# Kernel optimization log

Measured on AMD Instinct MI355X. Metric: run time of the kernel, lower is better.

## Reference

```python
import jax, jax.numpy as jnp
import numpy as np

EPS = 1e-5

def _quant_w(w):
    # symmetric per-tensor 8-bit weight quantization with straight-through estimator
    s = jnp.max(jnp.abs(w)) / 127.0
    wq = jnp.round(jnp.clip(w / s, -127.0, 127.0)) * s
    return w + jax.lax.stop_gradient(wq - w)

def _adder_conv(x, w, stride):
    # AdderNet conv: out[b,co,ow] = -sum_{cin,k} |x[b,cin,ow*stride+k] - w[co,cin,k]|
    # x: (B, Cin, L), w: (Co, Cin, K)
    B, Cin, L = x.shape
    Co, _, K = w.shape
    Ow = (L - K) // stride + 1
    idx = jnp.arange(Ow)[:, None] * stride + jnp.arange(K)[None, :]      # (Ow, K)
    patches = x[:, :, idx]                                               # (B, Cin, Ow, K)
    diff = jnp.abs(patches[:, None] - w[None, :, :, None, :])            # (B, Co, Cin, Ow, K)
    return -diff.sum(axis=(2, 4))                                        # (B, Co, Ow)

def _bn(x, p):
    # eval-mode BatchNorm; x: (B,C,W), p: (4,C) = [gamma, beta, running_mean, running_var]
    g, b, m, v = p
    return (x - m[:, None]) * (g[:, None] * jax.lax.rsqrt(v[:, None] + EPS)) + b[:, None]

def _bn_params(key, c):
    k1, k2, k3, k4 = jax.random.split(key, 4)
    g = jax.random.uniform(k1, (c,)) + 0.5
    b = 0.1 * jax.random.normal(k2, (c,))
    m = 0.1 * jax.random.normal(k3, (c,))
    v = jax.random.uniform(k4, (c,)) + 0.5
    return jnp.stack([g, b, m, v]).astype(jnp.float32)

def setup_inputs() -> dict:
    key = jax.random.key(0)
    ks = jax.random.split(key, 22)
    B = 8192
    w = lambda k, shp: (0.1 * jax.random.normal(k, shp)).astype(jnp.float32)
    return {
        'x': jax.random.normal(ks[0], (B, 1, 1, 256), dtype=jnp.float32),
        'w_pre1': w(ks[1], (5, 1, 13)),   'bn_pre1': _bn_params(ks[2], 5),
        'w_pre2': w(ks[3], (10, 5, 9)),   'bn_pre2': _bn_params(ks[4], 10),
        'w_r1':   w(ks[5], (10, 10, 1)),  'bn_r1':   _bn_params(ks[6], 10),
        'w_r2':   w(ks[7], (10, 10, 1)),  'bn_r2':   _bn_params(ks[8], 10),
        'w_o1a':  w(ks[9], (70, 140, 1)), 'bn_o1a':  _bn_params(ks[10], 70),
        'w_o1b':  w(ks[11], (30, 70, 1)), 'bn_o1b':  _bn_params(ks[12], 30),
        'w_o1c':  w(ks[13], (1, 30, 1)),  'bn_o1c':  _bn_params(ks[14], 1),
        'w_o2a':  w(ks[15], (70, 140, 1)),'bn_o2a':  _bn_params(ks[16], 70),
        'w_o2b':  w(ks[17], (30, 70, 1)), 'bn_o2b':  _bn_params(ks[18], 30),
        'w_o2c':  w(ks[19], (1, 30, 1)),  'bn_o2c':  _bn_params(ks[20], 1),
    }

def reference(x, w_pre1, bn_pre1, w_pre2, bn_pre2, w_r1, bn_r1, w_r2, bn_r2,
              w_o1a, bn_o1a, w_o1b, bn_o1b, w_o1c, bn_o1c,
              w_o2a, bn_o2a, w_o2b, bn_o2b, w_o2c, bn_o2c):
    relu = jax.nn.relu
    B = x.shape[0]
    h = x.reshape(B, 1, 256)                                  # height dim is 1 -> 1D
    h = relu(_bn(_adder_conv(h, _quant_w(w_pre1), 5), bn_pre1))   # (B,5,49)
    h = relu(_bn(_adder_conv(h, _quant_w(w_pre2), 3), bn_pre2))   # (B,10,14)
    # ResBlock
    t = relu(_bn(_adder_conv(h, _quant_w(w_r1), 1), bn_r1))
    t = _bn(_adder_conv(t, _quant_w(w_r2), 1), bn_r2)
    h = relu(t + h)                                           # (B,10,14)
    f = h.reshape(B, 140, 1)                                  # flatten to channels
    # O1 branch (amplitude-weighted average lifetime)
    a = relu(_bn(_adder_conv(f, _quant_w(w_o1a), 1), bn_o1a))
    a = relu(_bn(_adder_conv(a, _quant_w(w_o1b), 1), bn_o1b))
    a = relu(_bn(_adder_conv(a, _quant_w(w_o1c), 1), bn_o1c))
    tau_amp = a.reshape(-1)                                   # (B,)
    # O2 branch (intensity-weighted average lifetime)
    b = relu(_bn(_adder_conv(f, _quant_w(w_o2a), 1), bn_o2a))
    b = relu(_bn(_adder_conv(b, _quant_w(w_o2b), 1), bn_o2b))
    b = relu(_bn(_adder_conv(b, _quant_w(w_o2c), 1), bn_o2c))
    tau_inten = b.reshape(-1)                                 # (B,)
    return (tau_amp, tau_inten)
```

## Files before the change

### kernel.cpp

```cpp
#include <hip/hip_runtime.h>

#define TPB 256
#define EPB 8
#define H1S 246
#define ES  280

#define WQ1   0
#define WQ2   65
#define WR1Q  515
#define WR2Q  615
#define WCQ   715
#define WSB   779
#define SMALL_N 1253
#define WQAT  1280
#define WQBT  20880

#define SB_P1 0
#define SB_P2 10
#define SB_R1 30
#define SB_R2 50
#define SB_A1 70
#define SB_B1 210
#define SB_C1 270
#define SB_A2 272
#define SB_B2 412
#define SB_C2 472

#define GFOLD(bn, C, OFF)                                                     \
  if (tid < (C)) {                                                            \
    float gg = (bn)[tid], bb = (bn)[(C) + tid];                               \
    float mm = (bn)[2 * (C) + tid], vv = (bn)[3 * (C) + tid];                 \
    float sc = gg / sqrtf(vv + 1e-5f);                                        \
    sbp[(OFF) + tid] = sc;                                                    \
    sbp[(OFF) + (C) + tid] = bb - mm * sc;                                    \
  }

extern "C" __global__ __launch_bounds__(256)
void prep(const float* __restrict__ w1,  const float* __restrict__ bnp1,
          const float* __restrict__ w2,  const float* __restrict__ bnp2,
          const float* __restrict__ wr1, const float* __restrict__ bnr1,
          const float* __restrict__ wr2, const float* __restrict__ bnr2,
          const float* __restrict__ wa1, const float* __restrict__ bna1,
          const float* __restrict__ wb1, const float* __restrict__ bnb1,
          const float* __restrict__ wc1, const float* __restrict__ bnc1,
          const float* __restrict__ wa2, const float* __restrict__ bna2,
          const float* __restrict__ wb2, const float* __restrict__ bnb2,
          const float* __restrict__ wc2, const float* __restrict__ bnc2,
          float* __restrict__ ws)
{
  __shared__ float s_red[4];
  const int tid = threadIdx.x;
  const int b = blockIdx.x;

  if (b == 10) {
    float* sbp = ws + WSB;
    GFOLD(bnp1, 5, SB_P1)  GFOLD(bnp2, 10, SB_P2)
    GFOLD(bnr1, 10, SB_R1) GFOLD(bnr2, 10, SB_R2)
    GFOLD(bna1, 70, SB_A1) GFOLD(bnb1, 30, SB_B1) GFOLD(bnc1, 1, SB_C1)
    GFOLD(bna2, 70, SB_A2) GFOLD(bnb2, 30, SB_B2) GFOLD(bnc2, 1, SB_C2)
    return;
  }

  const float* src; int n; int mode; int rofs; float* dst = ws;
  int ofs = 0;
  switch (b) {
    case 0: src = w1;  ofs = WQ1;      n = 65;   mode = 0; rofs = 0;  break;
    case 1: src = w2;  ofs = WQ2;      n = 450;  mode = 0; rofs = 0;  break;
    case 2: src = wr1; ofs = WR1Q;     n = 100;  mode = 0; rofs = 0;  break;
    case 3: src = wr2; ofs = WR2Q;     n = 100;  mode = 0; rofs = 0;  break;
    case 4: src = wa1; ofs = WQAT;     n = 9800; mode = 1; rofs = 0;  break;
    case 5: src = wb1; ofs = WQBT;     n = 2100; mode = 2; rofs = 0;  break;
    case 6: src = wc1; ofs = WCQ;      n = 30;   mode = 0; rofs = 0;  break;
    case 7: src = wa2; ofs = WQAT;     n = 9800; mode = 1; rofs = 70; break;
    case 8: src = wb2; ofs = WQBT;     n = 2100; mode = 2; rofs = 30; break;
    default:src = wc2; ofs = WCQ + 32; n = 30;   mode = 0; rofs = 0;  break;
  }

  const int n4 = n >> 2;
  const float4* s4 = (const float4*)src;

  float m = 0.f;
  for (int i = tid; i < n4; i += 256) {
    float4 v = s4[i];
    m = fmaxf(m, fmaxf(fmaxf(fabsf(v.x), fabsf(v.y)),
                       fmaxf(fabsf(v.z), fabsf(v.w))));
  }
  for (int i = (n4 << 2) + tid; i < n; i += 256) m = fmaxf(m, fabsf(src[i]));
#pragma unroll
  for (int off = 32; off > 0; off >>= 1)
    m = fmaxf(m, __shfl_down(m, off, 64));
  if ((tid & 63) == 0) s_red[tid >> 6] = m;
  __syncthreads();
  m = fmaxf(fmaxf(s_red[0], s_red[1]), fmaxf(s_red[2], s_red[3]));

  const float s = m / 127.0f;
  auto qz = [&](float w) {
    return rintf(fminf(fmaxf(w / s, -127.f), 127.f)) * s;
  };

  if (mode == 0) {
    for (int i = tid; i < n4; i += 256) {
      float4 v = s4[i];
      int base = 4 * i;
      dst[ofs + base]     = qz(v.x);
      dst[ofs + base + 1] = qz(v.y);
      dst[ofs + base + 2] = qz(v.z);
      dst[ofs + base + 3] = qz(v.w);
    }
    for (int i = (n4 << 2) + tid; i < n; i += 256) dst[ofs + i] = qz(src[i]);
  } else if (mode == 1) {
    for (int i = tid; i < n4; i += 256) {
      float4 v = s4[i];
      int base = 4 * i;
      int r = base / 140 + rofs, c = base % 140;
      float4 q4;
      q4.x = qz(v.x); q4.y = qz(v.y); q4.z = qz(v.z); q4.w = qz(v.w);
      *(float4*)&dst[ofs + ((c >> 2) * 140 + r) * 4] = q4;
    }
  } else {
    for (int i = tid; i < n4; i += 256) {
      float4 v = s4[i];
      int base = 4 * i;
      float q[4] = {qz(v.x), qz(v.y), qz(v.z), qz(v.w)};
#pragma unroll
      for (int cpt = 0; cpt < 4; ++cpt) {
        int ii = base + cpt;
        int r = ii / 70 + rofs, c = ii % 70;
        dst[ofs + ((c >> 1) * 60 + r) * 2 + (c & 1)] = q[cpt];
      }
    }
  }
}

extern "C" __global__ __launch_bounds__(TPB, 4)
void taunet(const float* __restrict__ x, const float* __restrict__ ws,
            float* __restrict__ out, int B)
{
  __shared__ __align__(16) float s_h1[EPB * H1S];
  __shared__ __align__(16) float s_e[EPB * ES];
  __shared__ __align__(16) float s_small[SMALL_N];

  const int tid = threadIdx.x;
  const int g  = tid >> 5;
  const int l  = tid & 31;
  const int ln = tid & 63;
  const int wv = tid >> 6;
  const int gp = 2 * wv;
  const int elem = blockIdx.x * EPB + g;

  {
    const float4* w4p = (const float4*)ws;
    for (int i = ln; i < (SMALL_N >> 2); i += 64)
      *(float4*)&s_small[i * 4] = w4p[i];
    if (ln == 0) s_small[1252] = ws[1252];
  }

  {
    const float4* xb = (const float4*)x;
#pragma unroll
    for (int it = 0; it < 2; ++it) {
      int e = gp + it;
      int ge = blockIdx.x * EPB + e;
      if (ge < B) {
        float4 v = xb[ge * 64 + ln];
        *(float4*)&s_e[e * ES + ln * 4] = v;
      }
    }
  }

  const float* sb = &s_small[WSB];

  {
    const float* xe = &s_e[g * ES];
#pragma unroll
    for (int rep = 0; rep < 2; ++rep) {
      int p = l + 32 * rep;
      bool act = p < 49;
      int ps = act ? p : 0;
      float win[13];
#pragma unroll
      for (int k = 0; k < 13; ++k) win[k] = xe[5 * ps + k];
#pragma unroll
      for (int ci = 0; ci < 5; ++ci) {
        float a0 = 0.f, a1 = 0.f;
#pragma unroll
        for (int k = 0; k < 13; ++k) {
          float d = fabsf(win[k] - ws[WQ1 + ci * 13 + k]);
          if (k & 1) a1 += d; else a0 += d;
        }
        float v = fmaxf(fmaf(-(a0 + a1), ws[WSB + SB_P1 + ci],
                             ws[WSB + SB_P1 + 5 + ci]), 0.f);
        if (act) s_h1[g * H1S + ci * 49 + ps] = v;
      }
    }
  }

  {
    const int ch = l >> 4;
    const int ow16 = l & 15;
    const bool act = ow16 < 14;
    const int ow = act ? ow16 : 0;
    const float* h1b = &s_h1[g * H1S];
    float acc[5] = {0.f, 0.f, 0.f, 0.f, 0.f};
#pragma unroll
    for (int ci = 0; ci < 5; ++ci) {
      float w9[9];
#pragma unroll
      for (int k = 0; k < 9; ++k) w9[k] = h1b[ci * 49 + 3 * ow + k];
#pragma unroll
      for (int c = 0; c < 5; ++c) {
        int co = ch * 5 + c;
        float s0 = 0.f, s1 = 0.f;
#pragma unroll
        for (int k = 0; k < 9; ++k) {
          float d = fabsf(w9[k] - s_small[WQ2 + co * 45 + ci * 9 + k]);
          if (k & 1) s1 += d; else s0 += d;
        }
        acc[c] += s0 + s1;
      }
    }
#pragma unroll
    for (int c = 0; c < 5; ++c) {
      int co = ch * 5 + c;
      float v = fmaxf(fmaf(-acc[c], sb[SB_P2 + co], sb[SB_P2 + 10 + co]), 0.f);
      if (act) s_e[g * ES + co * 14 + ow] = v;
    }
  }

#pragma unroll
  for (int j = 0; j < 5; ++j) {
    int idx = l + 32 * j;
    if (idx < 140) {
      int co = idx / 14, ow = idx % 14;
      float a0 = 0.f, a1 = 0.f;
#pragma unroll
      for (int ci = 0; ci < 10; ++ci) {
        float d = fabsf(s_e[g * ES + ci * 14 + ow] - s_small[WR1Q + co * 10 + ci]);
        if (ci & 1) a1 += d; else a0 += d;
      }
      s_e[g * ES + 140 + idx] =
          fmaxf(fmaf(-(a0 + a1), sb[SB_R1 + co], sb[SB_R1 + 10 + co]), 0.f);
    }
  }

#pragma unroll
  for (int j = 0; j < 5; ++j) {
    int idx = l + 32 * j;
    if (idx < 140) {
      int co = idx / 14, ow = idx % 14;
      float a0 = 0.f, a1 = 0.f;
#pragma unroll
      for (int ci = 0; ci < 10; ++ci) {
        float d = fabsf(s_e[g * ES + 140 + ci * 14 + ow] - s_small[WR2Q + co * 10 + ci]);
        if (ci & 1) a1 += d; else a0 += d;
      }
      float t2 = fmaf(-(a0 + a1), sb[SB_R2 + co], sb[SB_R2 + 10 + co]);
      s_e[g * ES + idx] = fmaxf(t2 + s_e[g * ES + idx], 0.f);
    }
  }

  {
    const float* hb0 = &s_e[gp * ES];
    const float* hb1 = &s_e[(gp + 1) * ES];

    const int r01[2] = {ln, ln + 64};
    const bool s2a = ln < 12;
    const bool s2b = (ln >= 12) && (ln < 24);
    const int r2 = 128 + (s2a ? ln : (s2b ? ln - 12 : 0));

    float accA[2][4], accB[2][4], acc2[4];
#pragma unroll
    for (int p = 0; p < 2; ++p)
#pragma unroll
      for (int j = 0; j < 4; ++j) { accA[p][j] = 0.f; accB[p][j] = 0.f; }
#pragma unroll
    for (int j = 0; j < 4; ++j) acc2[j] = 0.f;

#pragma unroll 2
    for (int cb = 0; cb < 35; ++cb) {
      float4 h4 = *(const float4*)&hb0[cb * 4];
      float4 k4 = *(const float4*)&hb1[cb * 4];
      float4 p4;
      p4.x = s2a ? h4.x : k4.x;
      p4.y = s2a ? h4.y : k4.y;
      p4.z = s2a ? h4.z : k4.z;
      p4.w = s2a ? h4.w : k4.w;
#pragma unroll
      for (int p = 0; p < 2; ++p) {
        float4 w4 = *(const float4*)&ws[WQAT + (cb * 140 + r01[p]) * 4];
        accA[p][0] += fabsf(h4.x - w4.x);
        accA[p][1] += fabsf(h4.y - w4.y);
        accA[p][2] += fabsf(h4.z - w4.z);
        accA[p][3] += fabsf(h4.w - w4.w);
        accB[p][0] += fabsf(k4.x - w4.x);
        accB[p][1] += fabsf(k4.y - w4.y);
        accB[p][2] += fabsf(k4.z - w4.z);
        accB[p][3] += fabsf(k4.w - w4.w);
      }
      float4 w2v = *(const float4*)&ws[WQAT + (cb * 140 + r2) * 4];
      acc2[0] += fabsf(p4.x - w2v.x);
      acc2[1] += fabsf(p4.y - w2v.y);
      acc2[2] += fabsf(p4.z - w2v.z);
      acc2[3] += fabsf(p4.w - w2v.w);
    }
#pragma unroll
    for (int p = 0; p < 2; ++p) {
      int cl = r01[p];
      int co  = cl < 70 ? cl : cl - 70;
      int off = cl < 70 ? SB_A1 : SB_A2;
      float sc = sb[off + co], bi = sb[off + 70 + co];
      float sadA = (accA[p][0] + accA[p][1]) + (accA[p][2] + accA[p][3]);
      float sadB = (accB[p][0] + accB[p][1]) + (accB[p][2] + accB[p][3]);
      s_h1[gp * H1S + cl]       = fmaxf(fmaf(-sadA, sc, bi), 0.f);
      s_h1[(gp + 1) * H1S + cl] = fmaxf(fmaf(-sadB, sc, bi), 0.f);
    }
    if (s2a || s2b) {
      int cl = r2;
      int co = cl - 70;
      float sc = sb[SB_A2 + co], bi = sb[SB_A2 + 70 + co];
      float sad = (acc2[0] + acc2[1]) + (acc2[2] + acc2[3]);
      int e = s2a ? gp : (gp + 1);
      s_h1[e * H1S + cl] = fmaxf(fmaf(-sad, sc, bi), 0.f);
    }

    {
      bool act = ln < 60;
      int rl = act ? ln : 0;
      int br = rl >= 30;
      int co = br ? rl - 30 : rl;
      const float* h0 = &s_h1[gp * H1S + br * 70];
      const float* h1 = &s_h1[(gp + 1) * H1S + br * 70];
      int off = br ? SB_B2 : SB_B1;
      float a0 = 0.f, a1 = 0.f, b0 = 0.f, b1 = 0.f;
#pragma unroll 8
      for (int ci = 0; ci < 35; ++ci) {
        float2 w2v = *(const float2*)&ws[WQBT + (ci * 60 + rl) * 2];
        float2 hv0 = *(const float2*)&h0[2 * ci];
        float2 hv1 = *(const float2*)&h1[2 * ci];
        a0 += fabsf(hv0.x - w2v.x);
        a1 += fabsf(hv0.y - w2v.y);
        b0 += fabsf(hv1.x - w2v.x);
        b1 += fabsf(hv1.y - w2v.y);
      }
      if (act) {
        float sc = sb[off + co], bi = sb[off + 30 + co];
        s_e[gp * ES + 140 + rl]       = fmaxf(fmaf(-(a0 + a1), sc, bi), 0.f);
        s_e[(gp + 1) * ES + 140 + rl] = fmaxf(fmaf(-(b0 + b1), sc, bi), 0.f);
      }
    }

    for (int br = 0; br < 2; ++br) {
      float d = 0.f;
      if (l < 30)
        d = fabsf(s_e[g * ES + 140 + br * 30 + l] - s_small[WCQ + br * 32 + l]);
#pragma unroll
      for (int off = 16; off > 0; off >>= 1)
        d += __shfl_down(d, off, 32);
      if (l == 0 && elem < B) {
        int sbC = br ? SB_C2 : SB_C1;
        out[br * B + elem] = fmaxf(fmaf(-d, sb[sbC], sb[sbC + 1]), 0.f);
      }
    }
  }
}

extern "C" void kernel_launch(void* const* d_in, const int* in_sizes, int n_in,
                              void* d_out, int out_size, void* d_ws, size_t ws_size,
                              hipStream_t stream) {
  const float* x    = (const float*)d_in[0];
  const float* w1   = (const float*)d_in[1];
  const float* bnp1 = (const float*)d_in[2];
  const float* w2   = (const float*)d_in[3];
  const float* bnp2 = (const float*)d_in[4];
  const float* wr1  = (const float*)d_in[5];
  const float* bnr1 = (const float*)d_in[6];
  const float* wr2  = (const float*)d_in[7];
  const float* bnr2 = (const float*)d_in[8];
  const float* wa1  = (const float*)d_in[9];
  const float* bna1 = (const float*)d_in[10];
  const float* wb1  = (const float*)d_in[11];
  const float* bnb1 = (const float*)d_in[12];
  const float* wc1  = (const float*)d_in[13];
  const float* bnc1 = (const float*)d_in[14];
  const float* wa2  = (const float*)d_in[15];
  const float* bna2 = (const float*)d_in[16];
  const float* wb2  = (const float*)d_in[17];
  const float* bnb2 = (const float*)d_in[18];
  const float* wc2  = (const float*)d_in[19];
  const float* bnc2 = (const float*)d_in[20];

  float* ws = (float*)d_ws;
  int B = in_sizes[0] / 256;
  int blocks = (B + EPB - 1) / EPB;

  hipLaunchKernelGGL(prep, dim3(11), dim3(256), 0, stream,
                     w1, bnp1, w2, bnp2, wr1, bnr1, wr2, bnr2,
                     wa1, bna1, wb1, bnb1, wc1, bnc1,
                     wa2, bna2, wb2, bnb2, wc2, bnc2, ws);

  hipLaunchKernelGGL(taunet, dim3(blocks), dim3(TPB), 0, stream,
                     x, ws, (float*)d_out, B);
}
```

Measured before the change: 131.4 us.

## Read small weights from global memory with padded vector layout instead of LDS

Drops the per-block copy of small quantized weights and BN scale/bias into shared memory. The prep kernel now also writes stride-12 padded copies of the pre2 and residual weights, so the main kernel can fetch them straight from global (cached) memory with float4/float2 vector loads. This frees LDS, which may allow more blocks per CU, and removes the staging copy. It also precomputes each thread's channel and position indices for the residual loops. The cost is that weight reads now go through the cache path instead of LDS broadcast, with higher latency.

```diff
diff --git a/kernel.cpp b/kernel.cpp
--- a/kernel.cpp
+++ b/kernel.cpp
@@ -11,9 +11,11 @@
 #define WR2Q  615
 #define WCQ   715
 #define WSB   779
-#define SMALL_N 1253
 #define WQAT  1280
 #define WQBT  20880
+#define WQ2P  25080
+#define WR1P  25680
+#define WR2P  25800
 
 #define SB_P1 0
 #define SB_P2 10
@@ -63,11 +65,15 @@
 
   const float* src; int n; int mode; int rofs; float* dst = ws;
   int ofs = 0;
+  int pofs = -1; int pmode = 0;
   switch (b) {
     case 0: src = w1;  ofs = WQ1;      n = 65;   mode = 0; rofs = 0;  break;
-    case 1: src = w2;  ofs = WQ2;      n = 450;  mode = 0; rofs = 0;  break;
-    case 2: src = wr1; ofs = WR1Q;     n = 100;  mode = 0; rofs = 0;  break;
-    case 3: src = wr2; ofs = WR2Q;     n = 100;  mode = 0; rofs = 0;  break;
+    case 1: src = w2;  ofs = WQ2;      n = 450;  mode = 0; rofs = 0;
+            pofs = WQ2P; pmode = 1; break;
+    case 2: src = wr1; ofs = WR1Q;     n = 100;  mode = 0; rofs = 0;
+            pofs = WR1P; pmode = 2; break;
+    case 3: src = wr2; ofs = WR2Q;     n = 100;  mode = 0; rofs = 0;
+            pofs = WR2P; pmode = 2; break;
     case 4: src = wa1; ofs = WQAT;     n = 9800; mode = 1; rofs = 0;  break;
     case 5: src = wb1; ofs = WQBT;     n = 2100; mode = 2; rofs = 0;  break;
     case 6: src = wc1; ofs = WCQ;      n = 30;   mode = 0; rofs = 0;  break;
@@ -130,6 +136,22 @@
       }
     }
   }
+
+  if (pofs >= 0) {
+    for (int i = tid; i < n; i += 256) {
+      float q = qz(src[i]);
+      int di;
+      if (pmode == 1) {
+        int r = i / 45, cc = i - r * 45;
+        int ci = cc / 9, k = cc - ci * 9;
+        di = (r * 5 + ci) * 12 + k;
+      } else {
+        int r = i / 10, c = i - r * 10;
+        di = r * 12 + c;
+      }
+      dst[pofs + di] = q;
+    }
+  }
 }
 
 extern "C" __global__ __launch_bounds__(TPB, 4)
@@ -138,7 +160,6 @@
 {
   __shared__ __align__(16) float s_h1[EPB * H1S];
   __shared__ __align__(16) float s_e[EPB * ES];
-  __shared__ __align__(16) float s_small[SMALL_N];
 
   const int tid = threadIdx.x;
   const int g  = tid >> 5;
@@ -148,12 +169,7 @@
   const int gp = 2 * wv;
   const int elem = blockIdx.x * EPB + g;
 
-  {
-    const float4* w4p = (const float4*)ws;
-    for (int i = ln; i < (SMALL_N >> 2); i += 64)
-      *(float4*)&s_small[i * 4] = w4p[i];
-    if (ln == 0) s_small[1252] = ws[1252];
-  }
+  const float* sb = &ws[WSB];
 
   {
     const float4* xb = (const float4*)x;
@@ -167,8 +183,6 @@
       }
     }
   }
-
-  const float* sb = &s_small[WSB];
 
   {
     const float* xe = &s_e[g * ES];
@@ -210,12 +224,15 @@
 #pragma unroll
       for (int c = 0; c < 5; ++c) {
         int co = ch * 5 + c;
-        float s0 = 0.f, s1 = 0.f;
-#pragma unroll
-        for (int k = 0; k < 9; ++k) {
-          float d = fabsf(w9[k] - s_small[WQ2 + co * 45 + ci * 9 + k]);
-          if (k & 1) s1 += d; else s0 += d;
-        }
+        const float* wp = &ws[WQ2P + (co * 5 + ci) * 12];
+        float4 wa4 = *(const float4*)&wp[0];
+        float4 wb4 = *(const float4*)&wp[4];
+        float w8v = wp[8];
+        float s0 = fabsf(w9[0] - wa4.x) + fabsf(w9[2] - wa4.z) +
+                   fabsf(w9[4] - wb4.x) + fabsf(w9[6] - wb4.z) +
+                   fabsf(w9[8] - w8v);
+        float s1 = fabsf(w9[1] - wa4.y) + fabsf(w9[3] - wa4.w) +
+                   fabsf(w9[5] - wb4.y) + fabsf(w9[7] - wb4.w);
         acc[c] += s0 + s1;
       }
     }
@@ -227,17 +244,32 @@
     }
   }
 
+  int co5[5], ow5[5]; bool a5[5];
 #pragma unroll
   for (int j = 0; j < 5; ++j) {
     int idx = l + 32 * j;
-    if (idx < 140) {
-      int co = idx / 14, ow = idx % 14;
-      float a0 = 0.f, a1 = 0.f;
-#pragma unroll
-      for (int ci = 0; ci < 10; ++ci) {
-        float d = fabsf(s_e[g * ES + ci * 14 + ow] - s_small[WR1Q + co * 10 + ci]);
-        if (ci & 1) a1 += d; else a0 += d;
-      }
+    a5[j] = idx < 140;
+    int id2 = a5[j] ? idx : 0;
+    co5[j] = id2 / 14;
+    ow5[j] = id2 - co5[j] * 14;
+  }
+
+#pragma unroll
+  for (int j = 0; j < 5; ++j) {
+    if (a5[j]) {
+      int co = co5[j], ow = ow5[j];
+      int idx = l + 32 * j;
+      const float* wp = &ws[WR1P + co * 12];
+      float4 wa4 = *(const float4*)&wp[0];
+      float4 wb4 = *(const float4*)&wp[4];
+      float2 wc2 = *(const float2*)&wp[8];
+      const float* ip = &s_e[g * ES + ow];
+      float a0 = fabsf(ip[0]   - wa4.x) + fabsf(ip[28]  - wa4.z) +
+                 fabsf(ip[56]  - wb4.x) + fabsf(ip[84]  - wb4.z) +
+                 fabsf(ip[112] - wc2.x);
+      float a1 = fabsf(ip[14]  - wa4.y) + fabsf(ip[42]  - wa4.w) +
+                 fabsf(ip[70]  - wb4.y) + fabsf(ip[98]  - wb4.w) +
+                 fabsf(ip[126] - wc2.y);
       s_e[g * ES + 140 + idx] =
           fmaxf(fmaf(-(a0 + a1), sb[SB_R1 + co], sb[SB_R1 + 10 + co]), 0.f);
     }
@@ -245,15 +277,20 @@
 
 #pragma unroll
   for (int j = 0; j < 5; ++j) {
-    int idx = l + 32 * j;
-    if (idx < 140) {
-      int co = idx / 14, ow = idx % 14;
-      float a0 = 0.f, a1 = 0.f;
-#pragma unroll
-      for (int ci = 0; ci < 10; ++ci) {
-        float d = fabsf(s_e[g * ES + 140 + ci * 14 + ow] - s_small[WR2Q + co * 10 + ci]);
-        if (ci & 1) a1 += d; else a0 += d;
-      }
+    if (a5[j]) {
+      int co = co5[j], ow = ow5[j];
+      int idx = l + 32 * j;
+      const float* wp = &ws[WR2P + co * 12];
+      float4 wa4 = *(const float4*)&wp[0];
+      float4 wb4 = *(const float4*)&wp[4];
+      float2 wc2 = *(const float2*)&wp[8];
+      const float* ip = &s_e[g * ES + 140 + ow];
+      float a0 = fabsf(ip[0]   - wa4.x) + fabsf(ip[28]  - wa4.z) +
+                 fabsf(ip[56]  - wb4.x) + fabsf(ip[84]  - wb4.z) +
+                 fabsf(ip[112] - wc2.x);
+      float a1 = fabsf(ip[14]  - wa4.y) + fabsf(ip[42]  - wa4.w) +
+                 fabsf(ip[70]  - wb4.y) + fabsf(ip[98]  - wb4.w) +
+                 fabsf(ip[126] - wc2.y);
       float t2 = fmaf(-(a0 + a1), sb[SB_R2 + co], sb[SB_R2 + 10 + co]);
       s_e[g * ES + idx] = fmaxf(t2 + s_e[g * ES + idx], 0.f);
     }
@@ -352,7 +389,7 @@
     for (int br = 0; br < 2; ++br) {
       float d = 0.f;
       if (l < 30)
-        d = fabsf(s_e[g * ES + 140 + br * 30 + l] - s_small[WCQ + br * 32 + l]);
+        d = fabsf(s_e[g * ES + 140 + br * 30 + l] - ws[WCQ + br * 32 + l]);
 #pragma unroll
       for (int off = 16; off > 0; off >>= 1)
         d += __shfl_down(d, off, 32);
```

New measurement: 133.9 us. About the same (+1.9%).
